# Kernel optimization log

Measured on AMD Instinct MI355X. Metric: run time of the kernel, lower is better.

Reference implementation:

```python
import jax, jax.numpy as jnp
import numpy as np

# Dims: B batch, C=P channels (features per pixel), H*W=N pixels, M ELM models, Q=1 hidden units
M, Q, B, C, H, W_SP = 4, 1, 32, 1024, 28, 28
P = C
N = H * W_SP
EPS = 1e-10


def _lcg_weights(m, n, seed):
    """Deterministic LCG pseudo-random weights, z-score standardized (ELM_AE init)."""
    L = m * n
    a, b, c = L + 2, L + 3, float(L) ** 2
    v = np.zeros(L, dtype=np.float64)
    v[0] = seed + 1.0
    for i in range(1, L):
        v[i] = (a * v[i - 1] + b) % c
    v = (v - v.mean()) / (v.std() + EPS)
    return v.reshape(m, n).astype(np.float32)


def setup_inputs() -> dict:
    key = jax.random.key(0)
    x = jax.random.normal(key, (B, C, H, W_SP), dtype=jnp.float32)
    # One Q x P random input-weight matrix per ELM model, seed = model * (Q * P)
    Wm = jnp.stack([jnp.asarray(_lcg_weights(Q, P, model * (Q * P))) for model in range(M)])  # [M, Q, P]
    return {"x": x, "Wm": Wm}


def reference(x, Wm):
    b, c, h, w = x.shape
    # _norm('l2', ...): per-channel L2 normalization over (h, w), as F.normalize(dim=(1,2))
    norms = jnp.linalg.norm(x.reshape(b, c, h * w), axis=-1)[:, :, None, None]  # [B, C, 1, 1]
    xn = x / jnp.maximum(norms, EPS)
    X = xn.reshape(b, c, h * w)  # meta activation map per sample: [B, P, N]
    # ELM-AE hidden layer, batched over (sample, model): g = sigmoid(W @ X)
    G = jax.nn.sigmoid(jnp.einsum('mqp,bpn->bmqn', Wm, X))  # [B, M, Q, N]
    # fit_AE: output weights beta = pinv(g^T) @ X^T  -> [Q, P]
    pinvGt = jnp.linalg.pinv(jnp.swapaxes(G, -1, -2))       # [B, M, Q, N]
    beta = jnp.einsum('bmqn,bpn->bmqp', pinvGt, X)          # [B, M, Q, P]
    # sum over the M models; Q == 1 so flatten (Q, P) -> Q*P features
    feats = beta.sum(axis=1).reshape(b, -1)                 # [B, Q*P]
    return jnp.nan_to_num(feats)
```

## Files before the change

kernel.cpp:

```cpp
#include <hip/hip_runtime.h>
#include <math.h>

#define BATCH 32
#define CH    1024
#define NPix  784
#define MMOD  4
#define NPC   32
#define PPC   32
#define GCH   16
#define NF4   196
#define K1B   512

typedef __attribute__((ext_vector_type(4))) _Float16 half4;

__device__ __forceinline__ float wave_reduce(float s) {
    #pragma unroll
    for (int off = 32; off; off >>= 1) s += __shfl_down(s, off, 64);
    return s;
}

__device__ __forceinline__ float dpp_wave_sum(float v) {
    int x;
    x = __builtin_amdgcn_update_dpp(0, __builtin_bit_cast(int, v), 0x111, 0xf, 0xf, true);
    v += __builtin_bit_cast(float, x);
    x = __builtin_amdgcn_update_dpp(0, __builtin_bit_cast(int, v), 0x112, 0xf, 0xf, true);
    v += __builtin_bit_cast(float, x);
    x = __builtin_amdgcn_update_dpp(0, __builtin_bit_cast(int, v), 0x114, 0xf, 0xf, true);
    v += __builtin_bit_cast(float, x);
    x = __builtin_amdgcn_update_dpp(0, __builtin_bit_cast(int, v), 0x118, 0xf, 0xf, true);
    v += __builtin_bit_cast(float, x);
    x = __builtin_amdgcn_update_dpp(0, __builtin_bit_cast(int, v), 0x142, 0xa, 0xf, true);
    v += __builtin_bit_cast(float, x);
    x = __builtin_amdgcn_update_dpp(0, __builtin_bit_cast(int, v), 0x143, 0xc, 0xf, true);
    v += __builtin_bit_cast(float, x);
    return v;
}

__global__ __launch_bounds__(K1B) void k_nz(const float* __restrict__ x,
                                            const float* __restrict__ Wm,
                                            float* __restrict__ inv_norm,
                                            half4* __restrict__ zpart) {
    __shared__ float sq_l[PPC][4];
    __shared__ float4 wl4[PPC];
    __shared__ float4 zl[NF4][MMOD];
    const int blk = blockIdx.x;
    const int b  = blk >> 5;
    const int pc = blk & (NPC - 1);
    const int t = threadIdx.x;
    const int g = t >> 8;
    const int lt = t & 255;
    const int gwv = (t >> 6) & 3;
    const int lane = t & 63;
    const bool act = lt < NF4;
    const float4* xb4 = (const float4*)(x + ((size_t)b * CH + (size_t)pc * PPC) * NPix);
    const int tt = act ? lt : 0;

    float4 xv[GCH];
    #pragma unroll
    for (int pp = 0; pp < GCH; pp++)
        xv[pp] = xb4[(g * GCH + pp) * NF4 + tt];

    #pragma unroll
    for (int pp = 0; pp < GCH; pp++) {
        float4 v = xv[pp];
        float s = act ? (v.x*v.x + v.y*v.y + v.z*v.z + v.w*v.w) : 0.f;
        s = dpp_wave_sum(s);
        if (lane == 63) sq_l[g * GCH + pp][gwv] = s;
    }
    __syncthreads();

    if (t < PPC) {
        const float s = sq_l[t][0] + sq_l[t][1] + sq_l[t][2] + sq_l[t][3];
        const float inv = 1.f / fmaxf(sqrtf(s), 1e-10f);
        const int p = pc * PPC + t;
        inv_norm[b * CH + p] = inv;
        float4 w4;
        w4.x = Wm[0 * CH + p] * inv;
        w4.y = Wm[1 * CH + p] * inv;
        w4.z = Wm[2 * CH + p] * inv;
        w4.w = Wm[3 * CH + p] * inv;
        wl4[t] = w4;
    }
    __syncthreads();

    float4 a0 = {0,0,0,0}, a1 = {0,0,0,0}, a2 = {0,0,0,0}, a3 = {0,0,0,0};
    if (act) {
        #pragma unroll
        for (int pp = 0; pp < GCH; pp++) {
            const float4 w = wl4[g * GCH + pp];
            const float4 v = xv[pp];
            a0.x += w.x*v.x; a0.y += w.x*v.y; a0.z += w.x*v.z; a0.w += w.x*v.w;
            a1.x += w.y*v.x; a1.y += w.y*v.y; a1.z += w.y*v.z; a1.w += w.y*v.w;
            a2.x += w.z*v.x; a2.y += w.z*v.y; a2.z += w.z*v.z; a2.w += w.z*v.w;
            a3.x += w.w*v.x; a3.y += w.w*v.y; a3.z += w.w*v.z; a3.w += w.w*v.w;
        }
        if (g == 1) {
            zl[lt][0] = a0; zl[lt][1] = a1; zl[lt][2] = a2; zl[lt][3] = a3;
        }
    }
    __syncthreads();
    if (g == 0 && act) {
        float4 b0 = zl[lt][0], b1 = zl[lt][1], b2 = zl[lt][2], b3 = zl[lt][3];
        a0.x += b0.x; a0.y += b0.y; a0.z += b0.z; a0.w += b0.w;
        a1.x += b1.x; a1.y += b1.y; a1.z += b1.z; a1.w += b1.w;
        a2.x += b2.x; a2.y += b2.y; a2.z += b2.z; a2.w += b2.w;
        a3.x += b3.x; a3.y += b3.y; a3.z += b3.z; a3.w += b3.w;
        half4* zp = zpart + ((size_t)blk * MMOD) * NF4;
        half4 h0 = { (_Float16)a0.x, (_Float16)a0.y, (_Float16)a0.z, (_Float16)a0.w };
        half4 h1 = { (_Float16)a1.x, (_Float16)a1.y, (_Float16)a1.z, (_Float16)a1.w };
        half4 h2 = { (_Float16)a2.x, (_Float16)a2.y, (_Float16)a2.z, (_Float16)a2.w };
        half4 h3 = { (_Float16)a3.x, (_Float16)a3.y, (_Float16)a3.z, (_Float16)a3.w };
        zp[0 * NF4 + lt] = h0;
        zp[1 * NF4 + lt] = h1;
        zp[2 * NF4 + lt] = h2;
        zp[3 * NF4 + lt] = h3;
    }
}

__global__ __launch_bounds__(256) void k_gh(const half4* __restrict__ zpart,
                                            float* __restrict__ h) {
    __shared__ float red[4][MMOD];
    __shared__ float s2s[MMOD];
    const int b = blockIdx.x;
    const int t = threadIdx.x;
    const int wv = t >> 6, lane = t & 63;
    const bool act = t < NF4;
    const int tt = act ? t : 0;

    float4 g4[MMOD];
    #pragma unroll
    for (int m = 0; m < MMOD; m++) {
        float4 z = {0,0,0,0};
        #pragma unroll 8
        for (int pc = 0; pc < NPC; pc++) {
            half4 v = zpart[(((size_t)(b * NPC + pc)) * MMOD + m) * NF4 + tt];
            z.x += (float)v.x; z.y += (float)v.y; z.z += (float)v.z; z.w += (float)v.w;
        }
        float4 gg;
        gg.x = 1.f / (1.f + expf(-z.x));
        gg.y = 1.f / (1.f + expf(-z.y));
        gg.z = 1.f / (1.f + expf(-z.z));
        gg.w = 1.f / (1.f + expf(-z.w));
        if (!act) gg = (float4){0,0,0,0};
        g4[m] = gg;
        float s = dpp_wave_sum(gg.x*gg.x + gg.y*gg.y + gg.z*gg.z + gg.w*gg.w);
        if (lane == 63) red[wv][m] = s;
    }
    __syncthreads();
    if (t < MMOD) {
        float s = red[0][t] + red[1][t] + red[2][t] + red[3][t];
        s2s[t] = fmaxf(s, 1e-30f);
    }
    __syncthreads();
    if (act) {
        float4 hv = {0,0,0,0};
        #pragma unroll
        for (int m = 0; m < MMOD; m++) {
            const float r = 1.f / s2s[m];
            hv.x += g4[m].x * r; hv.y += g4[m].y * r;
            hv.z += g4[m].z * r; hv.w += g4[m].w * r;
        }
        ((float4*)(h + (size_t)b * NPix))[t] = hv;
    }
}

__global__ __launch_bounds__(256) void k_out(const float* __restrict__ x,
                                             const float* __restrict__ h,
                                             const float* __restrict__ inv_norm,
                                             float* __restrict__ out) {
    const int r = blockIdx.x * 4 + (threadIdx.x >> 6);
    const int lane = threadIdx.x & 63;
    const int b = r >> 10;
    const float4* x4 = (const float4*)(x + (size_t)r * NPix);
    const float4* h4 = (const float4*)(h + (size_t)b * NPix);
    float s = 0.f;
    #pragma unroll
    for (int i = 0; i < 3; i++) {
        float4 xv = x4[i * 64 + lane];
        float4 hv = h4[i * 64 + lane];
        s += xv.x*hv.x + xv.y*hv.y + xv.z*hv.z + xv.w*hv.w;
    }
    if (lane < 4) {
        float4 xv = x4[192 + lane];
        float4 hv = h4[192 + lane];
        s += xv.x*hv.x + xv.y*hv.y + xv.z*hv.z + xv.w*hv.w;
    }
    s = wave_reduce(s);
    if (lane == 0) {
        float v = s * inv_norm[r];
        if (!(v == v)) v = 0.f;
        v = fminf(fmaxf(v, -3.402823466e+38f), 3.402823466e+38f);
        out[r] = v;
    }
}

extern "C" void kernel_launch(void* const* d_in, const int* in_sizes, int n_in,
                              void* d_out, int out_size, void* d_ws, size_t ws_size,
                              hipStream_t stream) {
    const float* x  = (const float*)d_in[0];
    const float* Wm = (const float*)d_in[1];
    float* out = (float*)d_out;
    float* wsf = (float*)d_ws;

    float* inv_norm = wsf;
    float* h        = inv_norm + BATCH * CH;
    half4* zpart    = (half4*)(h + BATCH * NPix);

    k_nz<<<BATCH * NPC, K1B, 0, stream>>>(x, Wm, inv_norm, zpart);
    k_gh<<<BATCH, 256, 0, stream>>>(zpart, h);
    k_out<<<BATCH * CH / 4, 256, 0, stream>>>(x, h, inv_norm, out);
}
```

Before: 177.5 us.

## Split channel chunks into smaller blocks and store fp32 partial sums

Each k_nz block now handles 16 channels with 256 threads instead of 32 channels with 512 threads split into two groups. This removes the LDS cross-group reduction and one barrier, and the block count doubles. Partial projections are stored in fp32 instead of fp16, which restores accuracy. The cost is a much larger partial buffer that the 32-block k_gh kernel must read, with twice as many partials per batch.

Measured after the change: 190.2 us. 1.07x slower.

```diff
diff --git a/kernel.cpp b/kernel.cpp
--- a/kernel.cpp
+++ b/kernel.cpp
@@ -5,13 +5,10 @@
 #define CH    1024
 #define NPix  784
 #define MMOD  4
-#define NPC   32
-#define PPC   32
-#define GCH   16
+#define NPC   64
+#define PPC   16
+#define K1B   256
 #define NF4   196
-#define K1B   512
-
-typedef __attribute__((ext_vector_type(4))) _Float16 half4;
 
 __device__ __forceinline__ float wave_reduce(float s) {
     #pragma unroll
@@ -39,33 +36,28 @@
 __global__ __launch_bounds__(K1B) void k_nz(const float* __restrict__ x,
                                             const float* __restrict__ Wm,
                                             float* __restrict__ inv_norm,
-                                            half4* __restrict__ zpart) {
+                                            float* __restrict__ zpart) {
     __shared__ float sq_l[PPC][4];
     __shared__ float4 wl4[PPC];
-    __shared__ float4 zl[NF4][MMOD];
     const int blk = blockIdx.x;
-    const int b  = blk >> 5;
+    const int b  = blk >> 6;
     const int pc = blk & (NPC - 1);
     const int t = threadIdx.x;
-    const int g = t >> 8;
-    const int lt = t & 255;
-    const int gwv = (t >> 6) & 3;
-    const int lane = t & 63;
-    const bool act = lt < NF4;
+    const int wv = t >> 6, lane = t & 63;
+    const bool act = (t < NF4);
     const float4* xb4 = (const float4*)(x + ((size_t)b * CH + (size_t)pc * PPC) * NPix);
-    const int tt = act ? lt : 0;
+    const int tt = act ? t : 0;
 
-    float4 xv[GCH];
+    float4 xv[PPC];
     #pragma unroll
-    for (int pp = 0; pp < GCH; pp++)
-        xv[pp] = xb4[(g * GCH + pp) * NF4 + tt];
+    for (int pp = 0; pp < PPC; pp++) xv[pp] = xb4[pp * NF4 + tt];
 
     #pragma unroll
-    for (int pp = 0; pp < GCH; pp++) {
+    for (int pp = 0; pp < PPC; pp++) {
         float4 v = xv[pp];
         float s = act ? (v.x*v.x + v.y*v.y + v.z*v.z + v.w*v.w) : 0.f;
         s = dpp_wave_sum(s);
-        if (lane == 63) sq_l[g * GCH + pp][gwv] = s;
+        if (lane == 63) sq_l[pp][wv] = s;
     }
     __syncthreads();
 
@@ -83,41 +75,26 @@
     }
     __syncthreads();
 
-    float4 a0 = {0,0,0,0}, a1 = {0,0,0,0}, a2 = {0,0,0,0}, a3 = {0,0,0,0};
     if (act) {
+        float4 a0 = {0,0,0,0}, a1 = {0,0,0,0}, a2 = {0,0,0,0}, a3 = {0,0,0,0};
         #pragma unroll
-        for (int pp = 0; pp < GCH; pp++) {
-            const float4 w = wl4[g * GCH + pp];
+        for (int pp = 0; pp < PPC; pp++) {
+            const float4 w = wl4[pp];
             const float4 v = xv[pp];
             a0.x += w.x*v.x; a0.y += w.x*v.y; a0.z += w.x*v.z; a0.w += w.x*v.w;
             a1.x += w.y*v.x; a1.y += w.y*v.y; a1.z += w.y*v.z; a1.w += w.y*v.w;
             a2.x += w.z*v.x; a2.y += w.z*v.y; a2.z += w.z*v.z; a2.w += w.z*v.w;
             a3.x += w.w*v.x; a3.y += w.w*v.y; a3.z += w.w*v.z; a3.w += w.w*v.w;
         }
-        if (g == 1) {
-            zl[lt][0] = a0; zl[lt][1] = a1; zl[lt][2] = a2; zl[lt][3] = a3;
-        }
-    }
-    __syncthreads();
-    if (g == 0 && act) {
-        float4 b0 = zl[lt][0], b1 = zl[lt][1], b2 = zl[lt][2], b3 = zl[lt][3];
-        a0.x += b0.x; a0.y += b0.y; a0.z += b0.z; a0.w += b0.w;
-        a1.x += b1.x; a1.y += b1.y; a1.z += b1.z; a1.w += b1.w;
-        a2.x += b2.x; a2.y += b2.y; a2.z += b2.z; a2.w += b2.w;
-        a3.x += b3.x; a3.y += b3.y; a3.z += b3.z; a3.w += b3.w;
-        half4* zp = zpart + ((size_t)blk * MMOD) * NF4;
-        half4 h0 = { (_Float16)a0.x, (_Float16)a0.y, (_Float16)a0.z, (_Float16)a0.w };
-        half4 h1 = { (_Float16)a1.x, (_Float16)a1.y, (_Float16)a1.z, (_Float16)a1.w };
-        half4 h2 = { (_Float16)a2.x, (_Float16)a2.y, (_Float16)a2.z, (_Float16)a2.w };
-        half4 h3 = { (_Float16)a3.x, (_Float16)a3.y, (_Float16)a3.z, (_Float16)a3.w };
-        zp[0 * NF4 + lt] = h0;
-        zp[1 * NF4 + lt] = h1;
-        zp[2 * NF4 + lt] = h2;
-        zp[3 * NF4 + lt] = h3;
+        float4* zp = (float4*)(zpart + ((size_t)blk * MMOD) * NPix);
+        zp[0 * NF4 + t] = a0;
+        zp[1 * NF4 + t] = a1;
+        zp[2 * NF4 + t] = a2;
+        zp[3 * NF4 + t] = a3;
     }
 }
 
-__global__ __launch_bounds__(256) void k_gh(const half4* __restrict__ zpart,
+__global__ __launch_bounds__(256) void k_gh(const float* __restrict__ zpart,
                                             float* __restrict__ h) {
     __shared__ float red[4][MMOD];
     __shared__ float s2s[MMOD];
@@ -133,8 +110,8 @@
         float4 z = {0,0,0,0};
         #pragma unroll 8
         for (int pc = 0; pc < NPC; pc++) {
-            half4 v = zpart[(((size_t)(b * NPC + pc)) * MMOD + m) * NF4 + tt];
-            z.x += (float)v.x; z.y += (float)v.y; z.z += (float)v.z; z.w += (float)v.w;
+            float4 v = ((const float4*)(zpart + (((size_t)(b * NPC + pc)) * MMOD + m) * NPix))[tt];
+            z.x += v.x; z.y += v.y; z.z += v.z; z.w += v.w;
         }
         float4 gg;
         gg.x = 1.f / (1.f + expf(-z.x));
@@ -204,7 +181,7 @@
 
     float* inv_norm = wsf;
     float* h        = inv_norm + BATCH * CH;
-    half4* zpart    = (half4*)(h + BATCH * NPix);
+    float* zpart    = h + BATCH * NPix;
 
     k_nz<<<BATCH * NPC, K1B, 0, stream>>>(x, Wm, inv_norm, zpart);
     k_gh<<<BATCH, 256, 0, stream>>>(zpart, h);
```
